# Performance work log

Measured on AMD Instinct MI355X. Metric: run time of the kernel, lower is better.

The kernel has to match this reference:

```python
import jax, jax.numpy as jnp
import numpy as np

IN_FEAT = 78
C = 128          # out_channels
H = 8            # nheads (layer 1)
B = 1024         # num graphs / batch
NPG = 32         # nodes per graph
N = B * NPG      # total nodes
EPG = 128        # edges per graph
E = B * EPG
GENE = 18000
PROT = 6688
FP = 2048        # drr/drc fingerprint size
N_TASKS = 1


def _lin(key, fan_in, fan_out):
    kw, kb = jax.random.split(key)
    s = 1.0 / np.sqrt(fan_in)
    W = jax.random.uniform(kw, (fan_in, fan_out), jnp.float32, -s, s)
    b = jax.random.uniform(kb, (fan_out,), jnp.float32, -s, s)
    return W, b


def setup_inputs() -> dict:
    key = jax.random.key(0)
    ks = jax.random.split(key, 32)
    goff = jnp.repeat(jnp.arange(B, dtype=jnp.int64) * NPG, EPG)
    e1s = jax.random.randint(ks[0], (E,), 0, NPG, dtype=jnp.int64) + goff
    e1d = jax.random.randint(ks[1], (E,), 0, NPG, dtype=jnp.int64) + goff
    e2s = jax.random.randint(ks[2], (E,), 0, NPG, dtype=jnp.int64) + goff
    e2d = jax.random.randint(ks[3], (E,), 0, NPG, dtype=jnp.int64) + goff
    inp = {
        "x1": jax.random.normal(ks[4], (N, IN_FEAT), jnp.float32),
        "x2": jax.random.normal(ks[5], (N, IN_FEAT), jnp.float32),
        "gene_exp": jax.random.uniform(ks[6], (B, GENE), jnp.float32),
        "drr": jax.random.uniform(ks[7], (B, FP), jnp.float32),
        "drc": jax.random.uniform(ks[8], (B, FP), jnp.float32),
        "prot_exp": jax.random.normal(ks[9], (B, PROT), jnp.float32),
        "edge_index1": jnp.stack([e1s, e1d]),
        "edge_index2": jnp.stack([e2s, e2d]),
        "batch": jnp.repeat(jnp.arange(B, dtype=jnp.int64), NPG),
    }
    W1, b1 = _lin(ks[10], IN_FEAT, H * C)
    inp.update(W_gat1=W1, b_gat1=b1,
               a_src1=jax.random.normal(ks[11], (H, C), jnp.float32) * 0.1,
               a_dst1=jax.random.normal(ks[12], (H, C), jnp.float32) * 0.1)
    # GAT layer 2: 1024 -> 128, 1 head
    W2, b2 = _lin(ks[13], H * C, C)
    inp.update(W_gat2=W2, b_gat2=b2,
               a_src2=jax.random.normal(ks[14], (1, C), jnp.float32) * 0.1,
               a_dst2=jax.random.normal(ks[15], (1, C), jnp.float32) * 0.1)
    inp["W_fcg"], inp["b_fcg"] = _lin(ks[16], C, C)
    # reduction MLP: gene -> 2048 -> 512 -> 2C
    inp["Wr1"], inp["br1"] = _lin(ks[17], GENE, 2048)
    inp["Wr2"], inp["br2"] = _lin(ks[18], 2048, 512)
    inp["Wr3"], inp["br3"] = _lin(ks[19], 512, 2 * C)
    # prot MLP: 6688 -> 1024 -> 512 -> 2C
    inp["Wp1"], inp["bp1"] = _lin(ks[20], PROT, 1024)
    inp["Wp2"], inp["bp2"] = _lin(ks[21], 1024, 512)
    inp["Wp3"], inp["bp3"] = _lin(ks[22], 512, 2 * C)
    # fingerprint fusion linears
    inp["Wdrr"], inp["bdrr"] = _lin(ks[23], C + FP, C + FP)
    inp["Wdrc"], inp["bdrc"] = _lin(ks[24], C + FP, C + FP)
    # predictor (3 layers): in = 2*(C+FP) + 2C + 2C = 4864 -> 512 -> 256 -> n_tasks
    in_dim = 2 * (C + FP) + 2 * C + 2 * C
    inp["Wf1"], inp["bf1"] = _lin(ks[25], in_dim, 512)
    inp["Wf2"], inp["bf2"] = _lin(ks[26], 512, 256)
    inp["Wout"], inp["bout"] = _lin(ks[27], 256, N_TASKS)
    return inp


def _gat(x, src, dst, W, a_src, a_dst, b, heads, ch):
    n = x.shape[0]
    # add self-loops (PyG GATConv default)
    sl = jnp.arange(n, dtype=src.dtype)
    src = jnp.concatenate([src, sl])
    dst = jnp.concatenate([dst, sl])
    h = (x @ W).reshape(n, heads, ch)                    # [N,H,C]
    a_s = (h * a_src).sum(-1)                            # [N,H]
    a_d = (h * a_dst).sum(-1)
    e = jax.nn.leaky_relu(a_s[src] + a_d[dst], 0.2)      # [E',H]
    m = jax.ops.segment_max(e, dst, num_segments=n)
    ex = jnp.exp(e - m[dst])
    den = jax.ops.segment_sum(ex, dst, num_segments=n)
    alpha = ex / (den[dst] + 1e-16)
    out = jax.ops.segment_sum(h[src] * alpha[:, :, None], dst, num_segments=n)
    return out.reshape(n, heads * ch) + b


def reference(x1, x2, gene_exp, drr, drc, prot_exp,
              W_gat1, b_gat1, a_src1, a_dst1,
              W_gat2, b_gat2, a_src2, a_dst2,
              W_fcg, b_fcg,
              Wr1, br1, Wr2, br2, Wr3, br3,
              Wp1, bp1, Wp2, bp2, Wp3, bp3,
              Wdrr, bdrr, Wdrc, bdrc,
              Wf1, bf1, Wf2, bf2, Wout, bout,
              edge_index1, edge_index2, batch):
    nb = gene_exp.shape[0]

    def drug_branch(x, ei):
        x = jax.nn.elu(_gat(x, ei[0], ei[1], W_gat1, a_src1, a_dst1, b_gat1, H, C))
        x = jax.nn.elu(_gat(x, ei[0], ei[1], W_gat2, a_src2, a_dst2, b_gat2, 1, C))
        x = jax.ops.segment_max(x, batch, num_segments=nb)   # global max pool
        return jax.nn.relu(x @ W_fcg + b_fcg)

    g1 = drug_branch(x1, edge_index1)
    g2 = drug_branch(x2, edge_index2)

    # gene branch: L2 row-normalize then MLP (dropout off at inference)
    norm = jnp.sqrt((gene_exp * gene_exp).sum(1, keepdims=True))
    cell = gene_exp / jnp.maximum(norm, 1e-12)
    cell = jax.nn.relu(cell @ Wr1 + br1)
    cell = jax.nn.relu(cell @ Wr2 + br2)
    cell_vec = jax.nn.relu(cell @ Wr3 + br3)

    # protein branch
    p = prot_exp.reshape(-1, PROT)
    p = jax.nn.elu(p @ Wp1 + bp1)
    p = jax.nn.elu(p @ Wp2 + bp2)
    p = jax.nn.relu(p @ Wp3 + bp3)

    # fingerprint fusion
    d1 = jnp.concatenate([g1, drr], axis=1)
    d2 = jnp.concatenate([g2, drc], axis=1)
    d1 = jax.nn.relu(d1 @ Wdrr + bdrr)
    d2 = jax.nn.relu(d2 @ Wdrc + bdrc)

    y = jnp.concatenate([d1, d2, cell_vec, p], axis=1)
    # 3-layer predictor
    y = jax.nn.relu(y @ Wf1 + bf1)
    y = jax.nn.relu(y @ Wf2 + bf2)
    out = y @ Wout + bout
    return out
```

## Files before the change

### kernel.cpp

```cpp
#include <hip/hip_runtime.h>
#include <math.h>

#define BATCH   1024
#define NPG     32
#define NNODES  (BATCH * NPG)
#define EPG     128
#define INFEAT  78
#define CCH     128
#define NHEAD   8
#define GENE    18000
#define GENEP   18048
#define PROT    6688
#define PROTP   6784
#define FPD     2048

#define ACT_NONE 0
#define ACT_RELU 1
#define ACT_ELU  2

typedef unsigned short ushort_t;
typedef __bf16 bf16x8_t __attribute__((ext_vector_type(8)));
typedef float  f32x4_t  __attribute__((ext_vector_type(4)));

__device__ __forceinline__ float b2f(ushort_t u) {
    return __uint_as_float(((unsigned)u) << 16);
}
__device__ __forceinline__ ushort_t f2b(float f) {
    unsigned x = __float_as_uint(f);
    return (ushort_t)((x + 0x7fffu + ((x >> 16) & 1u)) >> 16);
}

#define GBM 128
#define GBN 128
#define GBK 32

__device__ __forceinline__ void gemm_core(
    const ushort_t* __restrict__ A, const ushort_t* __restrict__ BT,
    int K, int kb, int ke, int row0, int col0,
    ushort_t* Asl, ushort_t* Bsl, f32x4_t acc[4][4])
{
    const int tid  = threadIdx.x;
    const int wave = tid >> 6;
    const int lane = tid & 63;
    const int wr   = wave >> 1;
    const int wc   = wave & 1;
    const int srow = lane >> 2;
    const int skel = (lane & 3) * 8;

    for (int k0 = kb; k0 < ke; k0 += GBK) {
        __syncthreads();
        #pragma unroll
        for (int t = 0; t < 2; ++t) {
            const int rg = wave * 32 + t * 16;
            const ushort_t* ga = A + (size_t)(row0 + rg + srow) * K + k0 + skel;
            __builtin_amdgcn_global_load_lds(
                (const __attribute__((address_space(1))) void*)ga,
                (__attribute__((address_space(3))) void*)&Asl[rg * GBK], 16, 0, 0);
            const ushort_t* gb = BT + (size_t)(col0 + rg + srow) * K + k0 + skel;
            __builtin_amdgcn_global_load_lds(
                (const __attribute__((address_space(1))) void*)gb,
                (__attribute__((address_space(3))) void*)&Bsl[rg * GBK], 16, 0, 0);
        }
        __syncthreads();

        const int fr = lane & 15;
        const int fq = lane >> 4;
        bf16x8_t av[4], bv[4];
        #pragma unroll
        for (int i = 0; i < 4; ++i)
            av[i] = *(const bf16x8_t*)&Asl[(wr * 64 + i * 16 + fr) * GBK + fq * 8];
        #pragma unroll
        for (int j = 0; j < 4; ++j)
            bv[j] = *(const bf16x8_t*)&Bsl[(wc * 64 + j * 16 + fr) * GBK + fq * 8];
        #pragma unroll
        for (int i = 0; i < 4; ++i)
            #pragma unroll
            for (int j = 0; j < 4; ++j)
                acc[i][j] = __builtin_amdgcn_mfma_f32_16x16x32_bf16(
                    av[i], bv[j], acc[i][j], 0, 0, 0);
    }
}

__global__ __launch_bounds__(256) void gemm_bf16_kernel(
    const ushort_t* __restrict__ A, const ushort_t* __restrict__ BT,
    const float* __restrict__ bias, ushort_t* __restrict__ C,
    int M, int N, int K, int act)
{
    __shared__ ushort_t Asl[GBM * GBK];
    __shared__ ushort_t Bsl[GBN * GBK];
    const int lane = threadIdx.x & 63;
    const int wave = threadIdx.x >> 6;
    const int wr = wave >> 1, wc = wave & 1;
    const int row0 = blockIdx.y * GBM;
    const int col0 = blockIdx.x * GBN;

    f32x4_t acc[4][4] = {};
    gemm_core(A, BT, K, 0, K, row0, col0, Asl, Bsl, acc);

    const int fr = lane & 15;
    const int fq = lane >> 4;
    #pragma unroll
    for (int i = 0; i < 4; ++i) {
        #pragma unroll
        for (int j = 0; j < 4; ++j) {
            const int gn = col0 + wc * 64 + j * 16 + fr;
            const float bb = bias ? bias[gn] : 0.0f;
            #pragma unroll
            for (int r = 0; r < 4; ++r) {
                const int gm = row0 + wr * 64 + i * 16 + fq * 4 + r;
                float v = acc[i][j][r] + bb;
                if (act == ACT_RELU)     v = fmaxf(v, 0.0f);
                else if (act == ACT_ELU) v = (v > 0.0f) ? v : (expf(v) - 1.0f);
                C[(size_t)gm * N + gn] = f2b(v);
            }
        }
    }
}

__global__ __launch_bounds__(256) void gemm_bf16_part_kernel(
    const ushort_t* __restrict__ A, const ushort_t* __restrict__ BT,
    float* __restrict__ part, int M, int N, int K, int KC)
{
    __shared__ ushort_t Asl[GBM * GBK];
    __shared__ ushort_t Bsl[GBN * GBK];
    const int lane = threadIdx.x & 63;
    const int wave = threadIdx.x >> 6;
    const int wr = wave >> 1, wc = wave & 1;
    const int row0 = blockIdx.y * GBM;
    const int col0 = blockIdx.x * GBN;
    const int z    = blockIdx.z;
    const int kb   = z * KC;
    const int ke   = min(K, kb + KC);

    f32x4_t acc[4][4] = {};
    gemm_core(A, BT, K, kb, ke, row0, col0, Asl, Bsl, acc);

    const int fr = lane & 15;
    const int fq = lane >> 4;
    float* po = part + (size_t)z * M * N;
    #pragma unroll
    for (int i = 0; i < 4; ++i)
        #pragma unroll
        for (int j = 0; j < 4; ++j) {
            const int gn = col0 + wc * 64 + j * 16 + fr;
            #pragma unroll
            for (int r = 0; r < 4; ++r) {
                const int gm = row0 + wr * 64 + i * 16 + fq * 4 + r;
                po[(size_t)gm * N + gn] = acc[i][j][r];
            }
        }
}

__global__ __launch_bounds__(256) void reduce_kernel(
    const float* __restrict__ part, const float* __restrict__ bias,
    ushort_t* __restrict__ C, int MN, int N, int S, int act)
{
    int i4 = (blockIdx.x * 256 + threadIdx.x) * 4;
    if (i4 >= MN) return;
    float4 s = *(const float4*)&part[i4];
    for (int z = 1; z < S; ++z) {
        float4 v = *(const float4*)&part[(size_t)z * MN + i4];
        s.x += v.x; s.y += v.y; s.z += v.z; s.w += v.w;
    }
    const int n = i4 % N;
    float o[4] = { s.x, s.y, s.z, s.w };
    if (bias) { o[0] += bias[n]; o[1] += bias[n+1]; o[2] += bias[n+2]; o[3] += bias[n+3]; }
    unsigned pk[2];
    ushort_t r[4];
    #pragma unroll
    for (int k = 0; k < 4; ++k) {
        float v = o[k];
        if (act == ACT_RELU)     v = fmaxf(v, 0.0f);
        else if (act == ACT_ELU) v = (v > 0.0f) ? v : (expf(v) - 1.0f);
        r[k] = f2b(v);
    }
    pk[0] = (unsigned)r[0] | ((unsigned)r[1] << 16);
    pk[1] = (unsigned)r[2] | ((unsigned)r[3] << 16);
    *(uint2*)&C[i4] = make_uint2(pk[0], pk[1]);
}

#define DSREAD(dst, addr) asm volatile("ds_read_b128 %0, %1" : "=v"(dst) : "v"(addr))

template <int MH>
__device__ __forceinline__ void read_A8(bf16x8_t (&av)[4][2], unsigned b0, unsigned b1)
{
    DSREAD(av[0][0], b0 + (MH * 4 + 0) * 2048);
    DSREAD(av[0][1], b1 + (MH * 4 + 0) * 2048);
    DSREAD(av[1][0], b0 + (MH * 4 + 1) * 2048);
    DSREAD(av[1][1], b1 + (MH * 4 + 1) * 2048);
    DSREAD(av[2][0], b0 + (MH * 4 + 2) * 2048);
    DSREAD(av[2][1], b1 + (MH * 4 + 2) * 2048);
    DSREAD(av[3][0], b0 + (MH * 4 + 3) * 2048);
    DSREAD(av[3][1], b1 + (MH * 4 + 3) * 2048);
}

template <int NH>
__device__ __forceinline__ void read_B8(bf16x8_t (&bvh)[2][2], unsigned b0, unsigned b1)
{
    DSREAD(bvh[0][0], b0 + (NH * 2 + 0) * 2048);
    DSREAD(bvh[0][1], b1 + (NH * 2 + 0) * 2048);
    DSREAD(bvh[1][0], b0 + (NH * 2 + 1) * 2048);
    DSREAD(bvh[1][1], b1 + (NH * 2 + 1) * 2048);
}

template <int MH, int NH>
__device__ __forceinline__ void mfma_quad(const bf16x8_t (&av)[4][2],
                                          const bf16x8_t (&bvh)[2][2],
                                          f32x4_t (&acc)[8][4])
{
    #pragma unroll
    for (int qq = 0; qq < 4; ++qq)
        #pragma unroll
        for (int pp = 0; pp < 2; ++pp)
            #pragma unroll
            for (int ss = 0; ss < 2; ++ss)
                acc[MH * 4 + qq][NH * 2 + pp] = __builtin_amdgcn_mfma_f32_16x16x32_bf16(
                    av[qq][ss], bvh[pp][ss], acc[MH * 4 + qq][NH * 2 + pp], 0, 0, 0);
}

__device__ __forceinline__ void stage_half8(
    const ushort_t* __restrict__ G, int rc0, int K, int kt,
    unsigned lo0, ushort_t* smemp, int tid)
{
    const int lane = tid & 63;
    const int ce = (((lane & 7) ^ ((lane >> 3) & 7)) << 3);
    #pragma unroll
    for (int j = 0; j < 2; ++j) {
        const int rr = j * 64 + (tid >> 3);
        const ushort_t* g = G + (size_t)(rc0 + rr) * K + kt + ce;
        const unsigned lo = lo0 + (unsigned)((j * 64 + ((tid >> 3) & ~7)) * 128);
        __builtin_amdgcn_global_load_lds(
            (const __attribute__((address_space(1))) void*)g,
            (__attribute__((address_space(3))) void*)((char*)smemp + lo),
            16, 0, 0);
    }
}

#define PH_TAIL(MH, NH, BVH, VM) \
    __builtin_amdgcn_s_barrier(); \
    asm volatile("s_waitcnt lgkmcnt(0)"); \
    __builtin_amdgcn_sched_barrier(0); \
    __builtin_amdgcn_s_setprio(1); \
    mfma_quad<MH, NH>(av, BVH, acc); \
    __builtin_amdgcn_s_setprio(0); \
    __builtin_amdgcn_sched_barrier(0); \
    if (VM) asm volatile("s_waitcnt vmcnt(4)"); \
    __builtin_amdgcn_s_barrier();

__global__ __launch_bounds__(512, 2) void gemm_bf16_8ph_kernel(
    const ushort_t* __restrict__ A, const ushort_t* __restrict__ BT,
    float* __restrict__ part, int M, int N, int K, int IPC)
{
    extern __shared__ ushort_t smem8[];
    const int tid  = threadIdx.x;
    const int lane = tid & 63;
    const int wid  = tid >> 6;
    const int wm = wid >> 2, wn = wid & 3;
    const int fr = lane & 15, fq = lane >> 4;

    const int gx = N >> 8, gy = M >> 8;
    const int nwg = (int)gridDim.x;
    const int q8 = nwg >> 3, r8 = nwg & 7;
    const int xcd = (int)blockIdx.x & 7, sub = (int)blockIdx.x >> 3;
    const int wg = (xcd < r8 ? xcd * (q8 + 1) : r8 * (q8 + 1) + (xcd - r8) * q8) + sub;
    const int bz  = wg / (gx * gy);
    const int rem = wg - bz * gx * gy;
    const int by  = rem / gx;
    const int bx  = rem - by * gx;
    const int row0 = by << 8, col0 = bx << 8;

    const int iters = K >> 7;
    const int k0    = bz * IPC * 128;
    const int nit   = min(IPC, iters - bz * IPC);

    const unsigned SB  = (unsigned)(size_t)(__attribute__((address_space(3))) void*)smem8;
    const unsigned xa  = (unsigned)((fr & 7) << 4);
    const unsigned cs0 = ((unsigned)(fq * 16)) ^ xa;
    const unsigned cs1 = ((unsigned)(64 + fq * 16)) ^ xa;
    const unsigned arow = SB + (unsigned)((wm * 128 + fr) * 128);
    const unsigned brow = SB + 32768u + (unsigned)((wn * 64 + fr) * 128);

    f32x4_t  acc[8][4] = {};
    bf16x8_t av[4][2];
    bf16x8_t bv[2][2][2];

    auto KT = [&](int tt) { int kt = k0 + tt * 64; return kt > K - 64 ? K - 64 : kt; };
    auto STA = [&](int tt, int h) {
        stage_half8(A, row0 + h * 128, K, KT(tt),
                    (unsigned)(((tt & 1) * 65536) + h * 16384), smem8, tid);
    };
    auto STB = [&](int tt, int h) {
        stage_half8(BT, col0 + h * 128, K, KT(tt),
                    (unsigned)(((tt & 1) * 65536) + 32768 + h * 16384), smem8, tid);
    };

    STB(0, 0); STB(0, 1); STA(0, 0); STA(0, 1); STB(1, 0); STB(1, 1);
    asm volatile("s_waitcnt vmcnt(4)");
    __builtin_amdgcn_s_barrier();

    for (int it = 0; it < nit; ++it) {
        const int t = it << 1;
        read_A8<0>(av, arow + cs0, arow + cs1);
        read_B8<0>(bv[0], brow + cs0, brow + cs1);
        STA(t + 1, 0);
        PH_TAIL(0, 0, bv[0], 0)

        read_B8<1>(bv[1], brow + cs0, brow + cs1);
        STA(t + 1, 1);
        PH_TAIL(0, 1, bv[1], 0)

        read_A8<1>(av, arow + cs0, arow + cs1);
        STB(t + 2, 0);
        PH_TAIL(1, 0, bv[0], 0)

        STB(t + 2, 1);
        PH_TAIL(1, 1, bv[1], 1)

        read_A8<0>(av, arow + 65536u + cs0, arow + 65536u + cs1);
        read_B8<0>(bv[0], brow + 65536u + cs0, brow + 65536u + cs1);
        STA(t + 2, 0);
        PH_TAIL(0, 0, bv[0], 0)

        read_B8<1>(bv[1], brow + 65536u + cs0, brow + 65536u + cs1);
        STA(t + 2, 1);
        PH_TAIL(0, 1, bv[1], 0)

        read_A8<1>(av, arow + 65536u + cs0, arow + 65536u + cs1);
        STB(t + 3, 0);
        PH_TAIL(1, 0, bv[0], 0)

        STB(t + 3, 1);
        PH_TAIL(1, 1, bv[1], 1)
    }

    float* po = part + (size_t)bz * M * N;
    const int gmb = row0 + wm * 128 + fq * 4;
    const int gnb = col0 + wn * 64 + fr;
    #pragma unroll
    for (int mi = 0; mi < 8; ++mi)
        #pragma unroll
        for (int nj = 0; nj < 4; ++nj)
            #pragma unroll
            for (int r2 = 0; r2 < 4; ++r2)
                po[(size_t)(gmb + mi * 16 + r2) * N + (gnb + nj * 16)] = acc[mi][nj][r2];
}

__global__ __launch_bounds__(256) void cast_rows_kernel(
    const float* __restrict__ src, const float* __restrict__ rowscale,
    ushort_t* __restrict__ dst, int R, int Cin, int Cpad)
{
    int idx = blockIdx.x * 256 + threadIdx.x;
    if (idx >= R * Cpad) return;
    int r = idx / Cpad, c = idx - r * Cpad;
    float v = 0.0f;
    if (c < Cin) {
        v = src[(size_t)r * Cin + c];
        if (rowscale) v *= rowscale[r];
    }
    dst[idx] = f2b(v);
}

__global__ __launch_bounds__(256) void castT_kernel(
    const float* __restrict__ W, ushort_t* __restrict__ WT,
    int K, int N, int Kpad)
{
    __shared__ float t[32][33];
    const int nb = blockIdx.x * 32, kb = blockIdx.y * 32;
    const int x = threadIdx.x & 31, y = threadIdx.x >> 5;
    #pragma unroll
    for (int yy = 0; yy < 32; yy += 8) {
        int k = kb + y + yy, n = nb + x;
        t[y + yy][x] = (k < K && n < N) ? W[(size_t)k * N + n] : 0.0f;
    }
    __syncthreads();
    #pragma unroll
    for (int yy = 0; yy < 32; yy += 8) {
        int n = nb + y + yy, kk = kb + x;
        if (n < N && kk < Kpad) WT[(size_t)n * Kpad + kk] = f2b(t[x][y + yy]);
    }
}

__device__ __forceinline__ unsigned enc_f(float f) {
    unsigned u = __float_as_uint(f);
    return (u >> 31) ? ~u : (u | 0x80000000u);
}
__device__ __forceinline__ float dec_f(unsigned e) {
    return (e >> 31) ? __uint_as_float(e ^ 0x80000000u) : __uint_as_float(~e);
}

__device__ __forceinline__ unsigned swz32(int row, int chunk) {
    return (unsigned)((row << 6) + ((chunk ^ (row & 3)) << 4));
}

template <int POOL>
__global__ __launch_bounds__(256) void gat_fused_kernel(
    const ushort_t* __restrict__ h, const int* __restrict__ esrc,
    const int* __restrict__ edst, const float* __restrict__ a_src,
    const float* __restrict__ a_dst, const float* __restrict__ bias,
    ushort_t* __restrict__ out, int H)
{
    const int g    = blockIdx.x / H;
    const int hd   = blockIdx.x % H;
    const int tid  = threadIdx.x;
    const int lane = tid & 63;
    const int wave = tid >> 6;
    const int base = g * NPG;
    const int HC   = H * CCH;

    __shared__ __align__(16) char uni[NPG * CCH * 2];
    __shared__ __align__(16) ushort_t hT[CCH * 32];
    __shared__ float At[NPG][NPG];
    __shared__ float asv[CCH], adv[CCH];
    __shared__ float as_l[NPG], ad_l[NPG];
    __shared__ unsigned m_l[NPG];
    __shared__ float den_l[NPG];
    __shared__ float sc_l[EPG + NPG];
    __shared__ unsigned char s_l[EPG + NPG], d_l[EPG + NPG];

    ushort_t (*h_row)[CCH] = (ushort_t(*)[CCH])uni;
    ushort_t* AtH = (ushort_t*)uni;
    ushort_t* AtL = (ushort_t*)(uni + 2048);

    int es_r = 0, ed_r = 0;
    if (tid < EPG) {
        es_r = esrc[g * EPG + tid] - base;
        ed_r = edst[g * EPG + tid] - base;
    } else if (tid < EPG + NPG) {
        es_r = ed_r = tid - EPG;
    }

    {
        const int r4 = tid >> 6;
        const int cp = (tid & 63) * 2;
        #pragma unroll
        for (int rr = 0; rr < NPG; rr += 4) {
            const int r = rr + r4;
            unsigned v = *(const unsigned*)(h + (size_t)(base + r) * HC + hd * CCH + cp);
            *(unsigned*)&h_row[r][cp] = v;
        }
    }
    #pragma unroll
    for (int i = tid; i < NPG * NPG; i += 256) ((float*)At)[i] = 0.0f;
    if (tid < CCH) asv[tid] = a_src[hd * CCH + tid];
    else           adv[tid - CCH] = a_dst[hd * CCH + tid - CCH];
    if (tid < NPG) { m_l[tid] = 0u; den_l[tid] = 0.0f; }
    __syncthreads();

    for (int n = wave; n < NPG; n += 4) {
        float v0 = b2f(h_row[n][lane]), v1 = b2f(h_row[n][lane + 64]);
        float s = v0 * asv[lane] + v1 * asv[lane + 64];
        float d = v0 * adv[lane] + v1 * adv[lane + 64];
        #pragma unroll
        for (int o = 32; o > 0; o >>= 1) {
            s += __shfl_xor(s, o, 64);
            d += __shfl_xor(d, o, 64);
        }
        if (lane == 0) { as_l[n] = s; ad_l[n] = d; }
    }
    {
        const int c  = tid & 127;
        const int s0 = (tid >> 7) * 16;
        #pragma unroll
        for (int hh = 0; hh < 2; ++hh) {
            const int sb = s0 + hh * 8;
            unsigned pk[4];
            #pragma unroll
            for (int p = 0; p < 4; ++p) {
                unsigned lo = h_row[sb + 2 * p][c];
                unsigned hi = h_row[sb + 2 * p + 1][c];
                pk[p] = lo | (hi << 16);
            }
            *(uint4*)((char*)hT + swz32(c, sb >> 3)) = make_uint4(pk[0], pk[1], pk[2], pk[3]);
        }
    }
    __syncthreads();

    if (tid < EPG + NPG) {
        float e = as_l[es_r] + ad_l[ed_r];
        e = (e >= 0.0f) ? e : 0.2f * e;
        sc_l[tid] = e;
        s_l[tid] = (unsigned char)es_r;
        d_l[tid] = (unsigned char)ed_r;
        atomicMax(&m_l[ed_r], enc_f(e));
    }
    __syncthreads();

    if (tid < EPG + NPG) {
        float ex = expf(sc_l[tid] - dec_f(m_l[d_l[tid]]));
        sc_l[tid] = ex;
        atomicAdd(&den_l[d_l[tid]], ex);
    }
    __syncthreads();

    if (tid < EPG + NPG) {
        float al = sc_l[tid] / (den_l[d_l[tid]] + 1e-16f);
        atomicAdd(&At[s_l[tid]][d_l[tid]], al);
    }
    __syncthreads();

    {
        const int d  = tid >> 3;
        const int s4 = (tid & 7) * 4;
        float v0 = At[s4 + 0][d], v1 = At[s4 + 1][d];
        float v2 = At[s4 + 2][d], v3 = At[s4 + 3][d];
        ushort_t h0 = f2b(v0), h1 = f2b(v1), h2 = f2b(v2), h3 = f2b(v3);
        ushort_t l0 = f2b(v0 - b2f(h0)), l1 = f2b(v1 - b2f(h1));
        ushort_t l2 = f2b(v2 - b2f(h2)), l3 = f2b(v3 - b2f(h3));
        const unsigned a = swz32(d, s4 >> 3) + (unsigned)((s4 & 7) * 2);
        *(uint2*)((char*)AtH + a) = make_uint2((unsigned)h0 | ((unsigned)h1 << 16),
                                               (unsigned)h2 | ((unsigned)h3 << 16));
        *(uint2*)((char*)AtL + a) = make_uint2((unsigned)l0 | ((unsigned)l1 << 16),
                                               (unsigned)l2 | ((unsigned)l3 << 16));
    }
    __syncthreads();

    const int fr = lane & 15, fq = lane >> 4;
    const int dblk  = wave & 1;
    const int cbase = (wave >> 1) * 64;

    bf16x8_t aH = *(const bf16x8_t*)((char*)AtH + swz32(dblk * 16 + fr, fq));
    bf16x8_t aL = *(const bf16x8_t*)((char*)AtL + swz32(dblk * 16 + fr, fq));
    bf16x8_t bfr[4];
    #pragma unroll
    for (int q = 0; q < 4; ++q)
        bfr[q] = *(const bf16x8_t*)((char*)hT + swz32(cbase + q * 16 + fr, fq));

    f32x4_t acc[4] = {};
    #pragma unroll
    for (int q = 0; q < 4; ++q) {
        acc[q] = __builtin_amdgcn_mfma_f32_16x16x32_bf16(aH, bfr[q], acc[q], 0, 0, 0);
        acc[q] = __builtin_amdgcn_mfma_f32_16x16x32_bf16(aL, bfr[q], acc[q], 0, 0, 0);
    }

    if (POOL) {
        float* pool2 = (float*)At;
        #pragma unroll
        for (int q = 0; q < 4; ++q) {
            const int c = cbase + q * 16 + fr;
            const float bb = bias[hd * CCH + c];
            float m = -INFINITY;
            #pragma unroll
            for (int r = 0; r < 4; ++r) {
                float v = acc[q][r] + bb;
                v = (v > 0.0f) ? v : (expf(v) - 1.0f);
                m = fmaxf(m, v);
            }
            m = fmaxf(m, __shfl_xor(m, 16, 64));
            m = fmaxf(m, __shfl_xor(m, 32, 64));
            if (fq == 0) pool2[dblk * CCH + c] = m;
        }
        __syncthreads();
        if (tid < CCH)
            out[(size_t)g * CCH + tid] = f2b(fmaxf(pool2[tid], pool2[CCH + tid]));
    } else {
        #pragma unroll
        for (int q = 0; q < 4; ++q) {
            const int c = cbase + q * 16 + fr;
            const float bb = bias[hd * CCH + c];
            #pragma unroll
            for (int r = 0; r < 4; ++r) {
                const int d = dblk * 16 + fq * 4 + r;
                float v = acc[q][r] + bb;
                v = (v > 0.0f) ? v : (expf(v) - 1.0f);
                out[(size_t)(base + d) * HC + hd * CCH + c] = f2b(v);
            }
        }
    }
}

__global__ __launch_bounds__(256) void rownorm_kernel(
    const float* __restrict__ x, float* __restrict__ inv, int K)
{
    const int row = blockIdx.x;
    const int tid = threadIdx.x;
    const float* xp = x + (size_t)row * K;
    float s = 0.f;
    for (int k = tid; k < K; k += 256) { float v = xp[k]; s += v * v; }
    __shared__ float red[256];
    red[tid] = s;
    __syncthreads();
    for (int o = 128; o > 0; o >>= 1) {
        if (tid < o) red[tid] += red[tid + o];
        __syncthreads();
    }
    if (tid == 0) inv[row] = 1.0f / fmaxf(sqrtf(red[0]), 1e-12f);
}

__global__ __launch_bounds__(256) void copyb_kernel(
    ushort_t* __restrict__ dst, int ld, int off,
    const ushort_t* __restrict__ src, int rows, int cols)
{
    int idx = blockIdx.x * 256 + threadIdx.x;
    if (idx >= rows * cols) return;
    int r = idx / cols, c = idx - r * cols;
    dst[(size_t)r * ld + off + c] = src[idx];
}

__global__ __launch_bounds__(256) void castcols_kernel(
    ushort_t* __restrict__ dst, int ld, int off,
    const float* __restrict__ src, int rows, int cols)
{
    int idx = blockIdx.x * 256 + threadIdx.x;
    if (idx >= rows * cols) return;
    int r = idx / cols, c = idx - r * cols;
    dst[(size_t)r * ld + off + c] = f2b(src[idx]);
}

__global__ __launch_bounds__(256) void final_kernel(
    const ushort_t* __restrict__ y, const float* __restrict__ w,
    const float* __restrict__ b, float* __restrict__ out)
{
    const int row = blockIdx.x;
    const int tid = threadIdx.x;
    float v = b2f(y[(size_t)row * 256 + tid]) * w[tid];
    __shared__ float red[256];
    red[tid] = v;
    __syncthreads();
    for (int o = 128; o > 0; o >>= 1) {
        if (tid < o) red[tid] += red[tid + o];
        __syncthreads();
    }
    if (tid == 0) out[row] = red[0] + b[0];
}

static inline void launch_gemm(const ushort_t* A, const ushort_t* BT,
                               const float* bias, ushort_t* C,
                               int M, int N, int K, int act, hipStream_t stream)
{
    dim3 grid(N / GBN, M / GBM);
    gemm_bf16_kernel<<<grid, 256, 0, stream>>>(A, BT, bias, C, M, N, K, act);
}

static inline void launch_gemm_sk(const ushort_t* A, const ushort_t* BT,
                                  const float* bias, ushort_t* C, float* part,
                                  int M, int N, int K, int S, int act,
                                  hipStream_t stream)
{
    if (S <= 1) { launch_gemm(A, BT, bias, C, M, N, K, act, stream); return; }
    const int iters = K / GBK;
    const int ipc   = (iters + S - 1) / S;
    const int S_eff = (iters + ipc - 1) / ipc;
    const int KC    = ipc * GBK;
    dim3 grid(N / GBN, M / GBM, S_eff);
    gemm_bf16_part_kernel<<<grid, 256, 0, stream>>>(A, BT, part, M, N, K, KC);
    const int MN = M * N;
    reduce_kernel<<<(MN / 4 + 255) / 256, 256, 0, stream>>>(
        part, bias, C, MN, N, S_eff, act);
}

static inline void launch_gemm_8ph(const ushort_t* A, const ushort_t* BT,
                                   const float* bias, ushort_t* C, float* part,
                                   int M, int N, int K, int S, int act,
                                   hipStream_t stream)
{
    const int iters = K >> 7;
    const int ipc   = (iters + S - 1) / S;
    const int S_eff = (iters + ipc - 1) / ipc;
    const int gx = N >> 8, gy = M >> 8;
    const int nwg = gx * gy * S_eff;
    static bool attr_done = false;
    if (!attr_done) {
        (void)hipFuncSetAttribute((const void*)gemm_bf16_8ph_kernel,
                                  hipFuncAttributeMaxDynamicSharedMemorySize, 131072);
        attr_done = true;
    }
    gemm_bf16_8ph_kernel<<<dim3(nwg), 512, 131072, stream>>>(A, BT, part, M, N, K, ipc);
    const int MN = M * N;
    reduce_kernel<<<(MN / 4 + 255) / 256, 256, 0, stream>>>(
        part, bias, C, MN, N, S_eff, act);
}

static inline void launch_castT(const float* W, ushort_t* WT, int K, int N,
                                int Kpad, hipStream_t stream)
{
    dim3 grid((N + 31) / 32, (Kpad + 31) / 32);
    castT_kernel<<<grid, 256, 0, stream>>>(W, WT, K, N, Kpad);
}

extern "C" void kernel_launch(void* const* d_in, const int* in_sizes, int n_in,
                              void* d_out, int out_size, void* d_ws, size_t ws_size,
                              hipStream_t stream)
{
    const float* x1      = (const float*)d_in[0];
    const float* x2      = (const float*)d_in[1];
    const float* gene    = (const float*)d_in[2];
    const float* drr     = (const float*)d_in[3];
    const float* drc     = (const float*)d_in[4];
    const float* prot    = (const float*)d_in[5];
    const int*   ei1     = (const int*)d_in[6];
    const int*   ei2     = (const int*)d_in[7];
    const float* W_gat1  = (const float*)d_in[9];
    const float* b_gat1  = (const float*)d_in[10];
    const float* a_src1  = (const float*)d_in[11];
    const float* a_dst1  = (const float*)d_in[12];
    const float* W_gat2  = (const float*)d_in[13];
    const float* b_gat2  = (const float*)d_in[14];
    const float* a_src2  = (const float*)d_in[15];
    const float* a_dst2  = (const float*)d_in[16];
    const float* W_fcg   = (const float*)d_in[17];
    const float* b_fcg   = (const float*)d_in[18];
    const float* Wr1     = (const float*)d_in[19];
    const float* br1     = (const float*)d_in[20];
    const float* Wr2     = (const float*)d_in[21];
    const float* br2     = (const float*)d_in[22];
    const float* Wr3     = (const float*)d_in[23];
    const float* br3     = (const float*)d_in[24];
    const float* Wp1     = (const float*)d_in[25];
    const float* bp1     = (const float*)d_in[26];
    const float* Wp2     = (const float*)d_in[27];
    const float* bp2     = (const float*)d_in[28];
    const float* Wp3     = (const float*)d_in[29];
    const float* bp3     = (const float*)d_in[30];
    const float* Wdrr    = (const float*)d_in[31];
    const float* bdrr    = (const float*)d_in[32];
    const float* Wdrc    = (const float*)d_in[33];
    const float* bdrc    = (const float*)d_in[34];
    const float* Wf1     = (const float*)d_in[35];
    const float* bf1     = (const float*)d_in[36];
    const float* Wf2     = (const float*)d_in[37];
    const float* bf2     = (const float*)d_in[38];
    const float* Wout    = (const float*)d_in[39];
    const float* bout    = (const float*)d_in[40];
    float* outp = (float*)d_out;

    char* ws = (char*)d_ws;
    size_t off = 0;
    auto alloc = [&](size_t bytes) -> char* {
        char* r = ws + off;
        off += (bytes + 255) & ~(size_t)255;
        return r;
    };

    char* BIG0 = alloc(134217728);
    char* BIG1 = alloc(67108864);

    ushort_t* go1f   = (ushort_t*)BIG0;
    ushort_t* h1     = (ushort_t*)BIG1;
    float*    part   = (float*)BIG1;
    ushort_t* WT_r1  = (ushort_t*)(BIG0 + 0);
    ushort_t* gene_nb= (ushort_t*)(BIG0 + 73924608);
    ushort_t* cell1  = (ushort_t*)(BIG0 + 110886912);
    ushort_t* WT_r2  = (ushort_t*)(BIG0 + 115081216);
    ushort_t* WT_p2  = (ushort_t*)(BIG0 + 117178368);
    ushort_t* WT_p1  = (ushort_t*)(BIG0 + 118226944);

    ushort_t* xb     = (ushort_t*)alloc((size_t)NNODES * 96 * 2);
    char*     h2reg  = alloc((size_t)2 * NNODES * 128 * 2);
    char*     catreg = alloc((size_t)2 * 1024 * 2176 * 2);
    ushort_t* h2f    = (ushort_t*)h2reg;
    ushort_t* protb  = (ushort_t*)h2reg;
    ushort_t* cat1   = (ushort_t*)catreg;
    ushort_t* cat2   = (ushort_t*)(catreg + (size_t)1024 * 2176 * 2);
    ushort_t* pooled = (ushort_t*)alloc((size_t)2 * BATCH * 128 * 2);
    ushort_t* gpair  = (ushort_t*)alloc((size_t)2 * BATCH * 128 * 2);
    float*    invn   = (float*)alloc((size_t)BATCH * 4);
    ushort_t* cvec   = (ushort_t*)alloc((size_t)BATCH * 256 * 2);
    ushort_t* pvec   = (ushort_t*)alloc((size_t)BATCH * 256 * 2);
    ushort_t* y1     = (ushort_t*)alloc((size_t)BATCH * 512 * 2);
    ushort_t* y2     = (ushort_t*)alloc((size_t)BATCH * 256 * 2);
    ushort_t* WT_g1  = (ushort_t*)alloc((size_t)1024 * 96 * 2);
    ushort_t* WT_g2  = (ushort_t*)alloc((size_t)128 * 1024 * 2);
    ushort_t* WT_fcg = (ushort_t*)alloc((size_t)128 * 128 * 2);
    ushort_t* WT_r3  = (ushort_t*)alloc((size_t)256 * 512 * 2);
    ushort_t* WT_p3  = (ushort_t*)alloc((size_t)256 * 512 * 2);
    ushort_t* WT_f2  = (ushort_t*)alloc((size_t)256 * 512 * 2);
    ushort_t* WT_drr = (ushort_t*)alloc((size_t)2176 * 2176 * 2);
    ushort_t* WT_drc = (ushort_t*)alloc((size_t)2176 * 2176 * 2);
    ushort_t* WT_f1  = (ushort_t*)alloc((size_t)512 * 4864 * 2);
    ushort_t* p1b    = (ushort_t*)alloc((size_t)1024 * 1024 * 2);
    ushort_t* p2b    = (ushort_t*)alloc((size_t)1024 * 512 * 2);
    ushort_t* cell2  = (ushort_t*)alloc((size_t)1024 * 512 * 2);
    ushort_t* d1     = (ushort_t*)alloc((size_t)1024 * 2176 * 2);
    ushort_t* d2     = (ushort_t*)alloc((size_t)1024 * 2176 * 2);
    ushort_t* ybuf   = (ushort_t*)alloc((size_t)1024 * 4864 * 2);

    const int E = in_sizes[6] / 2;

    launch_castT(W_gat1, WT_g1, INFEAT, 1024, 96, stream);
    launch_castT(W_gat2, WT_g2, 1024, 128, 1024, stream);
    launch_castT(W_fcg,  WT_fcg, 128, 128, 128, stream);

    for (int drug = 0; drug < 2; drug++) {
        const float* x  = drug ? x2 : x1;
        const int*   es = (drug ? ei2 : ei1);
        const int*   ed = es + E;
        ushort_t* go1d = go1f + (size_t)drug * NNODES * 1024;

        cast_rows_kernel<<<(NNODES * 96 + 255) / 256, 256, 0, stream>>>(
            x, nullptr, xb, NNODES, INFEAT, 96);
        launch_gemm(xb, WT_g1, nullptr, h1, NNODES, 1024, 96, ACT_NONE, stream);
        gat_fused_kernel<0><<<BATCH * NHEAD, 256, 0, stream>>>(
            h1, es, ed, a_src1, a_dst1, b_gat1, go1d, NHEAD);
    }

    launch_gemm(go1f, WT_g2, nullptr, h2f, 2 * NNODES, 128, 1024, ACT_NONE, stream);

    launch_castT(Wr1, WT_r1, GENE, 2048, GENEP, stream);
    launch_castT(Wr2, WT_r2, 2048, 512, 2048, stream);
    launch_castT(Wp1, WT_p1, PROT, 1024, PROTP, stream);
    launch_castT(Wp2, WT_p2, 1024, 512, 1024, stream);
    launch_castT(Wr3, WT_r3, 512, 256, 512, stream);
    launch_castT(Wp3, WT_p3, 512, 256, 512, stream);
    launch_castT(Wf2, WT_f2, 512, 256, 512, stream);
    launch_castT(Wdrr, WT_drr, 2176, 2176, 2176, stream);
    launch_castT(Wdrc, WT_drc, 2176, 2176, 2176, stream);
    launch_castT(Wf1, WT_f1, 4864, 512, 4864, stream);

    for (int drug = 0; drug < 2; drug++) {
        const int* es = (drug ? ei2 : ei1);
        const int* ed = es + E;
        gat_fused_kernel<1><<<BATCH, 256, 0, stream>>>(
            h2f + (size_t)drug * NNODES * 128, es, ed,
            a_src2, a_dst2, b_gat2, pooled + (size_t)drug * BATCH * 128, 1);
    }
    launch_gemm(pooled, WT_fcg, b_fcg, gpair, 2 * BATCH, 128, 128, ACT_RELU, stream);

    rownorm_kernel<<<BATCH, 256, 0, stream>>>(gene, invn, GENE);
    cast_rows_kernel<<<(BATCH * GENEP + 255) / 256, 256, 0, stream>>>(
        gene, invn, gene_nb, BATCH, GENE, GENEP);
    launch_gemm_8ph(gene_nb, WT_r1, br1, cell1, part, BATCH, 2048, GENEP, 8, ACT_RELU, stream);
    launch_gemm_sk(cell1, WT_r2, br2, cell2, part, BATCH, 512, 2048, 8, ACT_RELU, stream);
    launch_gemm_sk(cell2, WT_r3, br3, cvec, part, BATCH, 256, 512, 4, ACT_RELU, stream);

    cast_rows_kernel<<<(BATCH * PROTP + 255) / 256, 256, 0, stream>>>(
        prot, nullptr, protb, BATCH, PROT, PROTP);
    launch_gemm_8ph(protb, WT_p1, bp1, p1b, part, BATCH, 1024, PROTP, 16, ACT_ELU, stream);
    launch_gemm_sk(p1b, WT_p2, bp2, p2b, part, BATCH, 512, 1024, 4, ACT_ELU, stream);
    launch_gemm_sk(p2b, WT_p3, bp3, pvec, part, BATCH, 256, 512, 4, ACT_RELU, stream);

    {
        int n = BATCH * CCH;
        copyb_kernel<<<(n + 255) / 256, 256, 0, stream>>>(cat1, 2176, 0, gpair, BATCH, CCH);
        copyb_kernel<<<(n + 255) / 256, 256, 0, stream>>>(cat2, 2176, 0, gpair + BATCH * CCH, BATCH, CCH);
        n = BATCH * FPD;
        castcols_kernel<<<(n + 255) / 256, 256, 0, stream>>>(cat1, 2176, CCH, drr, BATCH, FPD);
        castcols_kernel<<<(n + 255) / 256, 256, 0, stream>>>(cat2, 2176, CCH, drc, BATCH, FPD);
    }
    launch_gemm_sk(cat1, WT_drr, bdrr, d1, part, BATCH, 2176, 2176, 4, ACT_RELU, stream);
    launch_gemm_sk(cat2, WT_drc, bdrc, d2, part, BATCH, 2176, 2176, 4, ACT_RELU, stream);

    {
        int n = BATCH * 2176;
        copyb_kernel<<<(n + 255) / 256, 256, 0, stream>>>(ybuf, 4864, 0,    d1, BATCH, 2176);
        copyb_kernel<<<(n + 255) / 256, 256, 0, stream>>>(ybuf, 4864, 2176, d2, BATCH, 2176);
        n = BATCH * 256;
        copyb_kernel<<<(n + 255) / 256, 256, 0, stream>>>(ybuf, 4864, 4352, cvec, BATCH, 256);
        copyb_kernel<<<(n + 255) / 256, 256, 0, stream>>>(ybuf, 4864, 4608, pvec, BATCH, 256);
    }
    launch_gemm_sk(ybuf, WT_f1, bf1, y1, part, BATCH, 512, 4864, 8, ACT_RELU, stream);
    launch_gemm_sk(y1, WT_f2, bf2, y2, part, BATCH, 256, 512, 4, ACT_RELU, stream);
    final_kernel<<<BATCH, 256, 0, stream>>>(y2, Wout, bout, outp);
}
```

Before: 1.134 ms.

## Write GEMM epilogues into concat buffer, fuse rownorm+cast, vectorize GAT IO

The split-K reduce kernel now takes an output leading dimension and column offset, so the fingerprint, cell and protein GEMMs write straight into the concatenated predictor input and the separate copy kernels go away. The drr/drc GEMMs switch to the 8-phase GEMM with N padded to 2304 via zero-padded transposed weights. Row normalisation and bf16 casting of gene expression become one kernel. The GAT kernel loads and stores node rows with 16-byte vector accesses, staging output through LDS for coalesced writes. The padding adds wasted GEMM columns and the staged store adds an extra barrier.

```diff
diff --git a/kernel.cpp b/kernel.cpp
--- a/kernel.cpp
+++ b/kernel.cpp
@@ -153,30 +153,31 @@
 
 __global__ __launch_bounds__(256) void reduce_kernel(
     const float* __restrict__ part, const float* __restrict__ bias,
-    ushort_t* __restrict__ C, int MN, int N, int S, int act)
+    ushort_t* __restrict__ C, int MN, int N, int S, int act,
+    int Nb, int Cld, int Coff)
 {
     int i4 = (blockIdx.x * 256 + threadIdx.x) * 4;
     if (i4 >= MN) return;
+    const int r = i4 / N, n = i4 - r * N;
+    if (n >= Nb) return;
     float4 s = *(const float4*)&part[i4];
     for (int z = 1; z < S; ++z) {
         float4 v = *(const float4*)&part[(size_t)z * MN + i4];
         s.x += v.x; s.y += v.y; s.z += v.z; s.w += v.w;
     }
-    const int n = i4 % N;
     float o[4] = { s.x, s.y, s.z, s.w };
     if (bias) { o[0] += bias[n]; o[1] += bias[n+1]; o[2] += bias[n+2]; o[3] += bias[n+3]; }
-    unsigned pk[2];
-    ushort_t r[4];
+    ushort_t rr[4];
     #pragma unroll
     for (int k = 0; k < 4; ++k) {
         float v = o[k];
         if (act == ACT_RELU)     v = fmaxf(v, 0.0f);
         else if (act == ACT_ELU) v = (v > 0.0f) ? v : (expf(v) - 1.0f);
-        r[k] = f2b(v);
-    }
-    pk[0] = (unsigned)r[0] | ((unsigned)r[1] << 16);
-    pk[1] = (unsigned)r[2] | ((unsigned)r[3] << 16);
-    *(uint2*)&C[i4] = make_uint2(pk[0], pk[1]);
+        rr[k] = f2b(v);
+    }
+    unsigned pk0 = (unsigned)rr[0] | ((unsigned)rr[1] << 16);
+    unsigned pk1 = (unsigned)rr[2] | ((unsigned)rr[3] << 16);
+    *(uint2*)&C[(size_t)r * Cld + Coff + n] = make_uint2(pk0, pk1);
 }
 
 #define DSREAD(dst, addr) asm volatile("ds_read_b128 %0, %1" : "=v"(dst) : "v"(addr))
@@ -360,9 +361,40 @@
     dst[idx] = f2b(v);
 }
 
+__global__ __launch_bounds__(256) void rownorm_cast_kernel(
+    const float* __restrict__ x, ushort_t* __restrict__ dst, int K, int Kpad)
+{
+    const int row = blockIdx.x;
+    const int tid = threadIdx.x;
+    const float4* xp = (const float4*)(x + (size_t)row * K);
+    const int K4  = K >> 2;
+    const int Kp4 = Kpad >> 2;
+    float s = 0.f;
+    for (int k = tid; k < K4; k += 256) {
+        float4 v = xp[k];
+        s += v.x * v.x + v.y * v.y + v.z * v.z + v.w * v.w;
+    }
+    __shared__ float red[256];
+    red[tid] = s;
+    __syncthreads();
+    for (int o = 128; o > 0; o >>= 1) {
+        if (tid < o) red[tid] += red[tid + o];
+        __syncthreads();
+    }
+    const float inv = 1.0f / fmaxf(sqrtf(red[0]), 1e-12f);
+    ushort_t* dp = dst + (size_t)row * Kpad;
+    for (int k = tid; k < Kp4; k += 256) {
+        float4 v = (k < K4) ? xp[k] : make_float4(0.f, 0.f, 0.f, 0.f);
+        ushort_t r0 = f2b(v.x * inv), r1 = f2b(v.y * inv);
+        ushort_t r2 = f2b(v.z * inv), r3 = f2b(v.w * inv);
+        *(uint2*)&dp[k * 4] = make_uint2((unsigned)r0 | ((unsigned)r1 << 16),
+                                         (unsigned)r2 | ((unsigned)r3 << 16));
+    }
+}
+
 __global__ __launch_bounds__(256) void castT_kernel(
     const float* __restrict__ W, ushort_t* __restrict__ WT,
-    int K, int N, int Kpad)
+    int K, int N, int Kpad, int Npad)
 {
     __shared__ float t[32][33];
     const int nb = blockIdx.x * 32, kb = blockIdx.y * 32;
@@ -376,7 +408,8 @@
     #pragma unroll
     for (int yy = 0; yy < 32; yy += 8) {
         int n = nb + y + yy, kk = kb + x;
-        if (n < N && kk < Kpad) WT[(size_t)n * Kpad + kk] = f2b(t[x][y + yy]);
+        if (n < Npad && kk < Kpad)
+            WT[(size_t)n * Kpad + kk] = (n < N) ? f2b(t[x][y + yy]) : (ushort_t)0;
     }
 }
 
@@ -429,15 +462,14 @@
         es_r = ed_r = tid - EPG;
     }
 
+    const int srow = tid >> 3;
+    const int sch  = (tid & 7) * 16;
     {
-        const int r4 = tid >> 6;
-        const int cp = (tid & 63) * 2;
-        #pragma unroll
-        for (int rr = 0; rr < NPG; rr += 4) {
-            const int r = rr + r4;
-            unsigned v = *(const unsigned*)(h + (size_t)(base + r) * HC + hd * CCH + cp);
-            *(unsigned*)&h_row[r][cp] = v;
-        }
+        const ushort_t* src = h + (size_t)(base + srow) * HC + hd * CCH + sch;
+        uint4 v0 = *(const uint4*)(src);
+        uint4 v1 = *(const uint4*)(src + 8);
+        *(uint4*)&h_row[srow][sch]     = v0;
+        *(uint4*)&h_row[srow][sch + 8] = v1;
     }
     #pragma unroll
     for (int i = tid; i < NPG * NPG; i += 256) ((float*)At)[i] = 0.0f;
@@ -524,6 +556,8 @@
     #pragma unroll
     for (int q = 0; q < 4; ++q)
         bfr[q] = *(const bf16x8_t*)((char*)hT + swz32(cbase + q * 16 + fr, fq));
+
+    if (!POOL) __syncthreads();
 
     f32x4_t acc[4] = {};
     #pragma unroll
@@ -553,47 +587,33 @@
         if (tid < CCH)
             out[(size_t)g * CCH + tid] = f2b(fmaxf(pool2[tid], pool2[CCH + tid]));
     } else {
+        ushort_t (*o_l)[CCH] = (ushort_t(*)[CCH])hT;
         #pragma unroll
         for (int q = 0; q < 4; ++q) {
             const int c = cbase + q * 16 + fr;
             const float bb = bias[hd * CCH + c];
             #pragma unroll
             for (int r = 0; r < 4; ++r) {
-                const int d = dblk * 16 + fq * 4 + r;
                 float v = acc[q][r] + bb;
                 v = (v > 0.0f) ? v : (expf(v) - 1.0f);
-                out[(size_t)(base + d) * HC + hd * CCH + c] = f2b(v);
+                o_l[dblk * 16 + fq * 4 + r][c] = f2b(v);
             }
         }
-    }
-}
-
-__global__ __launch_bounds__(256) void rownorm_kernel(
-    const float* __restrict__ x, float* __restrict__ inv, int K)
-{
-    const int row = blockIdx.x;
-    const int tid = threadIdx.x;
-    const float* xp = x + (size_t)row * K;
-    float s = 0.f;
-    for (int k = tid; k < K; k += 256) { float v = xp[k]; s += v * v; }
-    __shared__ float red[256];
-    red[tid] = s;
-    __syncthreads();
-    for (int o = 128; o > 0; o >>= 1) {
-        if (tid < o) red[tid] += red[tid + o];
         __syncthreads();
-    }
-    if (tid == 0) inv[row] = 1.0f / fmaxf(sqrtf(red[0]), 1e-12f);
+        ushort_t* dst = out + (size_t)(base + srow) * HC + hd * CCH + sch;
+        *(uint4*)(dst)     = *(const uint4*)&o_l[srow][sch];
+        *(uint4*)(dst + 8) = *(const uint4*)&o_l[srow][sch + 8];
+    }
 }
 
 __global__ __launch_bounds__(256) void copyb_kernel(
-    ushort_t* __restrict__ dst, int ld, int off,
-    const ushort_t* __restrict__ src, int rows, int cols)
+    ushort_t* __restrict__ dst, int dld, int doff,
+    const ushort_t* __restrict__ src, int sld, int rows, int cols)
 {
     int idx = blockIdx.x * 256 + threadIdx.x;
     if (idx >= rows * cols) return;
     int r = idx / cols, c = idx - r * cols;
-    dst[(size_t)r * ld + off + c] = src[idx];
+    dst[(size_t)r * dld + doff + c] = src[(size_t)r * sld + c];
 }
 
 __global__ __launch_bounds__(256) void castcols_kernel(
@@ -634,9 +654,11 @@
 static inline void launch_gemm_sk(const ushort_t* A, const ushort_t* BT,
                                   const float* bias, ushort_t* C, float* part,
                                   int M, int N, int K, int S, int act,
-                                  hipStream_t stream)
-{
-    if (S <= 1) { launch_gemm(A, BT, bias, C, M, N, K, act, stream); return; }
+                                  hipStream_t stream,
+                                  int Nb = -1, int Cld = -1, int Coff = 0)
+{
+    if (Nb  < 0) Nb  = N;
+    if (Cld < 0) Cld = N;
     const int iters = K / GBK;
     const int ipc   = (iters + S - 1) / S;
     const int S_eff = (iters + ipc - 1) / ipc;
@@ -645,14 +667,17 @@
     gemm_bf16_part_kernel<<<grid, 256, 0, stream>>>(A, BT, part, M, N, K, KC);
     const int MN = M * N;
     reduce_kernel<<<(MN / 4 + 255) / 256, 256, 0, stream>>>(
-        part, bias, C, MN, N, S_eff, act);
+        part, bias, C, MN, N, S_eff, act, Nb, Cld, Coff);
 }
 
 static inline void launch_gemm_8ph(const ushort_t* A, const ushort_t* BT,
                                    const float* bias, ushort_t* C, float* part,
                                    int M, int N, int K, int S, int act,
-                                   hipStream_t stream)
-{
+                                   hipStream_t stream,
+                                   int Nb = -1, int Cld = -1, int Coff = 0)
+{
+    if (Nb  < 0) Nb  = N;
+    if (Cld < 0) Cld = N;
     const int iters = K >> 7;
     const int ipc   = (iters + S - 1) / S;
     const int S_eff = (iters + ipc - 1) / ipc;
@@ -667,14 +692,15 @@
     gemm_bf16_8ph_kernel<<<dim3(nwg), 512, 131072, stream>>>(A, BT, part, M, N, K, ipc);
     const int MN = M * N;
     reduce_kernel<<<(MN / 4 + 255) / 256, 256, 0, stream>>>(
-        part, bias, C, MN, N, S_eff, act);
+        part, bias, C, MN, N, S_eff, act, Nb, Cld, Coff);
 }
 
 static inline void launch_castT(const float* W, ushort_t* WT, int K, int N,
-                                int Kpad, hipStream_t stream)
-{
-    dim3 grid((N + 31) / 32, (Kpad + 31) / 32);
-    castT_kernel<<<grid, 256, 0, stream>>>(W, WT, K, N, Kpad);
+                                int Kpad, hipStream_t stream, int Npad = -1)
+{
+    if (Npad < 0) Npad = N;
+    dim3 grid((Npad + 31) / 32, (Kpad + 31) / 32);
+    castT_kernel<<<grid, 256, 0, stream>>>(W, WT, K, N, Kpad, Npad);
 }
 
 extern "C" void kernel_launch(void* const* d_in, const int* in_sizes, int n_in,
@@ -753,9 +779,6 @@
     ushort_t* cat2   = (ushort_t*)(catreg + (size_t)1024 * 2176 * 2);
     ushort_t* pooled = (ushort_t*)alloc((size_t)2 * BATCH * 128 * 2);
     ushort_t* gpair  = (ushort_t*)alloc((size_t)2 * BATCH * 128 * 2);
-    float*    invn   = (float*)alloc((size_t)BATCH * 4);
-    ushort_t* cvec   = (ushort_t*)alloc((size_t)BATCH * 256 * 2);
-    ushort_t* pvec   = (ushort_t*)alloc((size_t)BATCH * 256 * 2);
     ushort_t* y1     = (ushort_t*)alloc((size_t)BATCH * 512 * 2);
     ushort_t* y2     = (ushort_t*)alloc((size_t)BATCH * 256 * 2);
     ushort_t* WT_g1  = (ushort_t*)alloc((size_t)1024 * 96 * 2);
@@ -764,14 +787,12 @@
     ushort_t* WT_r3  = (ushort_t*)alloc((size_t)256 * 512 * 2);
     ushort_t* WT_p3  = (ushort_t*)alloc((size_t)256 * 512 * 2);
     ushort_t* WT_f2  = (ushort_t*)alloc((size_t)256 * 512 * 2);
-    ushort_t* WT_drr = (ushort_t*)alloc((size_t)2176 * 2176 * 2);
-    ushort_t* WT_drc = (ushort_t*)alloc((size_t)2176 * 2176 * 2);
+    ushort_t* WT_drr = (ushort_t*)alloc((size_t)2304 * 2176 * 2);
+    ushort_t* WT_drc = (ushort_t*)alloc((size_t)2304 * 2176 * 2);
     ushort_t* WT_f1  = (ushort_t*)alloc((size_t)512 * 4864 * 2);
     ushort_t* p1b    = (ushort_t*)alloc((size_t)1024 * 1024 * 2);
     ushort_t* p2b    = (ushort_t*)alloc((size_t)1024 * 512 * 2);
     ushort_t* cell2  = (ushort_t*)alloc((size_t)1024 * 512 * 2);
-    ushort_t* d1     = (ushort_t*)alloc((size_t)1024 * 2176 * 2);
-    ushort_t* d2     = (ushort_t*)alloc((size_t)1024 * 2176 * 2);
     ushort_t* ybuf   = (ushort_t*)alloc((size_t)1024 * 4864 * 2);
 
     const int E = in_sizes[6] / 2;
@@ -802,8 +823,8 @@
     launch_castT(Wr3, WT_r3, 512, 256, 512, stream);
     launch_castT(Wp3, WT_p3, 512, 256, 512, stream);
     launch_castT(Wf2, WT_f2, 512, 256, 512, stream);
-    launch_castT(Wdrr, WT_drr, 2176, 2176, 2176, stream);
-    launch_castT(Wdrc, WT_drc, 2176, 2176, 2176, stream);
+    launch_castT(Wdrr, WT_drr, 2176, 2176, 2176, stream, 2304);
+    launch_castT(Wdrc, WT_drc, 2176, 2176, 2176, stream, 2304);
     launch_castT(Wf1, WT_f1, 4864, 512, 4864, stream);
 
     for (int drug = 0; drug < 2; drug++) {
@@ -815,38 +836,32 @@
     }
     launch_gemm(pooled, WT_fcg, b_fcg, gpair, 2 * BATCH, 128, 128, ACT_RELU, stream);
 
-    rownorm_kernel<<<BATCH, 256, 0, stream>>>(gene, invn, GENE);
-    cast_rows_kernel<<<(BATCH * GENEP + 255) / 256, 256, 0, stream>>>(
-        gene, invn, gene_nb, BATCH, GENE, GENEP);
+    rownorm_cast_kernel<<<BATCH, 256, 0, stream>>>(gene, gene_nb, GENE, GENEP);
     launch_gemm_8ph(gene_nb, WT_r1, br1, cell1, part, BATCH, 2048, GENEP, 8, ACT_RELU, stream);
     launch_gemm_sk(cell1, WT_r2, br2, cell2, part, BATCH, 512, 2048, 8, ACT_RELU, stream);
-    launch_gemm_sk(cell2, WT_r3, br3, cvec, part, BATCH, 256, 512, 4, ACT_RELU, stream);
+    launch_gemm_sk(cell2, WT_r3, br3, ybuf, part, BATCH, 256, 512, 4, ACT_RELU, stream,
+                   256, 4864, 4352);
 
     cast_rows_kernel<<<(BATCH * PROTP + 255) / 256, 256, 0, stream>>>(
         prot, nullptr, protb, BATCH, PROT, PROTP);
     launch_gemm_8ph(protb, WT_p1, bp1, p1b, part, BATCH, 1024, PROTP, 16, ACT_ELU, stream);
     launch_gemm_sk(p1b, WT_p2, bp2, p2b, part, BATCH, 512, 1024, 4, ACT_ELU, stream);
-    launch_gemm_sk(p2b, WT_p3, bp3, pvec, part, BATCH, 256, 512, 4, ACT_RELU, stream);
+    launch_gemm_sk(p2b, WT_p3, bp3, ybuf, part, BATCH, 256, 512, 4, ACT_RELU, stream,
+                   256, 4864, 4608);
 
     {
         int n = BATCH * CCH;
-        copyb_kernel<<<(n + 255) / 256, 256, 0, stream>>>(cat1, 2176, 0, gpair, BATCH, CCH);
-        copyb_kernel<<<(n + 255) / 256, 256, 0, stream>>>(cat2, 2176, 0, gpair + BATCH * CCH, BATCH, CCH);
+        copyb_kernel<<<(n + 255) / 256, 256, 0, stream>>>(cat1, 2176, 0, gpair, 128, BATCH, CCH);
+        copyb_kernel<<<(n + 255) / 256, 256, 0, stream>>>(cat2, 2176, 0, gpair + BATCH * CCH, 128, BATCH, CCH);
         n = BATCH * FPD;
         castcols_kernel<<<(n + 255) / 256, 256, 0, stream>>>(cat1, 2176, CCH, drr, BATCH, FPD);
         castcols_kernel<<<(n + 255) / 256, 256, 0, stream>>>(cat2, 2176, CCH, drc, BATCH, FPD);
     }
-    launch_gemm_sk(cat1, WT_drr, bdrr, d1, part, BATCH, 2176, 2176, 4, ACT_RELU, stream);
-    launch_gemm_sk(cat2, WT_drc, bdrc, d2, part, BATCH, 2176, 2176, 4, ACT_RELU, stream);
-
-    {
-        int n = BATCH * 2176;
-        copyb_kernel<<<(n + 255) / 256, 256, 0, stream>>>(ybuf, 4864, 0,    d1, BATCH, 2176);
-        copyb_kernel<<<(n + 255) / 256, 256, 0, stream>>>(ybuf, 4864, 2176, d2, BATCH, 2176);
-        n = BATCH * 256;
-        copyb_kernel<<<(n + 255) / 256, 256, 0, stream>>>(ybuf, 4864, 4352, cvec, BATCH, 256);
-        copyb_kernel<<<(n + 255) / 256, 256, 0, stream>>>(ybuf, 4864, 4608, pvec, BATCH, 256);
-    }
+    launch_gemm_8ph(cat1, WT_drr, bdrr, ybuf, part, BATCH, 2304, 2176, 7, ACT_RELU, stream,
+                    2176, 4864, 0);
+    launch_gemm_8ph(cat2, WT_drc, bdrc, ybuf, part, BATCH, 2304, 2176, 7, ACT_RELU, stream,
+                    2176, 4864, 2176);
+
     launch_gemm_sk(ybuf, WT_f1, bf1, y1, part, BATCH, 512, 4864, 8, ACT_RELU, stream);
     launch_gemm_sk(y1, WT_f2, bf2, y2, part, BATCH, 256, 512, 4, ACT_RELU, stream);
     final_kernel<<<BATCH, 256, 0, stream>>>(y2, Wout, bout, outp);
```

After: 1.082 ms. -4.6%, faster.
